# Kernel tuning notes

Hardware: AMD Instinct MI355X
Metric: run time of the kernel (lower is better)

Reference implementation:

```python
import jax, jax.numpy as jnp
import numpy as np
import math

B, S = 512, 100
L, U = 50000, 2000
D, LOC_DIM, USER_DIM, TEMP_DIM = 80, 56, 12, 12
NHEAD, DFF = 4, 160


def _pe(seq_len, d):
    pos = np.arange(seq_len, dtype=np.float32)[:, None]
    div = np.exp(np.arange(0, d, 2, dtype=np.float32) * (-math.log(10000.0) / d))
    pe = np.zeros((seq_len, d), dtype=np.float32)
    pe[:, 0::2] = np.sin(pos * div)
    pe[:, 1::2] = np.cos(pos * div)
    return jnp.asarray(pe)


def _ln(x, g, b, eps=1e-5):
    m = x.mean(-1, keepdims=True)
    v = ((x - m) ** 2).mean(-1, keepdims=True)
    return (x - m) * jax.lax.rsqrt(v + eps) * g + b


def setup_inputs():
    key = jax.random.key(0)
    ks = jax.random.split(key, 16)
    f32 = jnp.float32
    def n(k, shape, s):
        return (jax.random.normal(k, shape) * s).astype(f32)
    return {
        'loc_seq': jax.random.randint(ks[0], (B, S), 0, L),
        'user_seq': jax.random.randint(ks[1], (B, S), 0, U),
        'weekday_seq': jax.random.randint(ks[2], (B, S), 0, 7),
        'start_min_seq': (jax.random.uniform(ks[3], (B, S)) * 1440.0).astype(f32),
        'dur_seq': (jax.random.uniform(ks[4], (B, S)) * 120.0).astype(f32),
        'diff_seq': jax.random.randint(ks[5], (B, S), 0, 7),
        'mask': jnp.ones((B, S), dtype=bool),
        'loc_emb': n(ks[6], (L, LOC_DIM), 0.01).at[0].set(0.0),
        'user_emb': n(ks[7], (U, USER_DIM), 0.01).at[0].set(0.0),
        'Wt': n(ks[8], (6, TEMP_DIM), 0.3), 'bt': jnp.zeros((TEMP_DIM,), f32),
        'in_g': jnp.ones((D,), f32), 'in_b': jnp.zeros((D,), f32),
        'Wq': n(ks[9], (D, D), 0.05), 'bq': jnp.zeros((D,), f32),
        'Wk': n(ks[10], (D, D), 0.05), 'bk': jnp.zeros((D,), f32),
        'Wv': n(ks[11], (D, D), 0.05), 'bv': jnp.zeros((D,), f32),
        'Wo': n(ks[12], (D, D), 0.05), 'bo': jnp.zeros((D,), f32),
        'ln1_g': jnp.ones((D,), f32), 'ln1_b': jnp.zeros((D,), f32),
        'W1': n(ks[13], (D, DFF), 0.05), 'b1': jnp.zeros((DFF,), f32),
        'W2': n(ks[14], (DFF, D), 0.05), 'b2': jnp.zeros((D,), f32),
        'ln2_g': jnp.ones((D,), f32), 'ln2_b': jnp.zeros((D,), f32),
        'out_g': jnp.ones((D,), f32), 'out_b': jnp.zeros((D,), f32),
        'Wp': n(ks[15], (D, L), 0.05), 'bp': jnp.zeros((L,), f32),
        'recency_decay': jnp.array(0.62, f32),
        'freq_weight': jnp.array(2.2, f32),
        'history_scale': jnp.array(11.0, f32),
        'model_weight': jnp.array(0.22, f32),
    }


def reference(loc_seq, user_seq, weekday_seq, start_min_seq, dur_seq, diff_seq, mask,
              loc_emb, user_emb, Wt, bt, in_g, in_b,
              Wq, bq, Wk, bk, Wv, bv, Wo, bo, ln1_g, ln1_b,
              W1, b1, W2, b2, ln2_g, ln2_b, out_g, out_b, Wp, bp,
              recency_decay, freq_weight, history_scale, model_weight):
    b, s = loc_seq.shape
    nloc = Wp.shape[1]
    valid = mask.astype(jnp.float32)
    # --- history scores: the torch per-timestep scatter loop, vectorized ---
    t = jnp.arange(s)
    rec_w = recency_decay ** (s - 1 - t).astype(jnp.float32)      # (s,) decay^time_from_end
    bidx = jnp.broadcast_to(jnp.arange(b)[:, None], (b, s))
    recency = jnp.zeros((b, nloc), jnp.float32).at[bidx, loc_seq].max(rec_w[None, :] * valid)
    freq = jnp.zeros((b, nloc), jnp.float32).at[bidx, loc_seq].add(valid)
    freq = freq / jnp.maximum(freq.max(axis=1, keepdims=True), 1.0)
    history_scores = history_scale * (recency + freq_weight * freq)
    # --- embeddings & temporal features ---
    time_rad = start_min_seq / 60.0 / 24.0 * 2.0 * math.pi
    wd_rad = weekday_seq.astype(jnp.float32) / 7.0 * 2.0 * math.pi
    feats = jnp.stack([jnp.sin(time_rad), jnp.cos(time_rad), jnp.log1p(dur_seq) / 8.0,
                       jnp.sin(wd_rad), jnp.cos(wd_rad), diff_seq.astype(jnp.float32) / 7.0], axis=-1)
    x = jnp.concatenate([loc_emb[loc_seq], user_emb[user_seq], feats @ Wt + bt], axis=-1)
    x = _ln(x, in_g, in_b) + _pe(s, x.shape[-1])[None]
    # --- 1-layer post-norm transformer encoder, erf-gelu, eval (no dropout) ---
    dh = D // NHEAD
    q = (x @ Wq + bq).reshape(b, s, NHEAD, dh)
    k = (x @ Wk + bk).reshape(b, s, NHEAD, dh)
    v = (x @ Wv + bv).reshape(b, s, NHEAD, dh)
    scores = jnp.einsum('bqhd,bkhd->bhqk', q, k) / math.sqrt(dh)
    scores = jnp.where(mask[:, None, None, :], scores, -1e9)
    attn = jnp.einsum('bhqk,bkhd->bqhd', jax.nn.softmax(scores, axis=-1), v).reshape(b, s, D)
    x = _ln(x + attn @ Wo + bo, ln1_g, ln1_b)
    x = _ln(x + jax.nn.gelu(x @ W1 + b1, approximate=False) @ W2 + b2, ln2_g, ln2_b)
    # --- gather last valid position ---
    last_idx = mask.sum(axis=1) - 1
    last = jnp.take_along_axis(x, last_idx[:, None, None], axis=1)[:, 0]
    last = _ln(last, out_g, out_b)
    learned = jax.nn.softmax(last @ Wp + bp, axis=1) * nloc
    return history_scores + model_weight * learned
```

## Files before the change

kernel.cpp:

```cpp
#include <hip/hip_runtime.h>
#include <hip/hip_bf16.h>
#include <math.h>

#define B 512
#define S 100
#define L 50000
#define D 80
#define NHEAD 4
#define DH 20
#define DFF 160
#define NTOK (B*S)
#define NTILES 3125

typedef __attribute__((ext_vector_type(8))) short bf16x8v;
typedef __attribute__((ext_vector_type(4))) float f32x4v;
typedef __attribute__((ext_vector_type(4))) unsigned short u16x4;
typedef __attribute__((ext_vector_type(8))) unsigned short u16x8;

__device__ __forceinline__ unsigned short f2bf(float f) {
    unsigned int x = __float_as_uint(f);
    unsigned int r = (x + 0x7FFFu + ((x >> 16) & 1u)) >> 16;
    return (unsigned short)r;
}

__device__ __forceinline__ float bf2f(unsigned short u) {
    return __uint_as_float(((unsigned int)u) << 16);
}

__device__ __forceinline__ float pe_val(int s, int d) {
    int k = d >> 1;
    float ang = (float)s * expf(-0.23025850929940458f * (float)k);
    return (d & 1) ? cosf(ang) : sinf(ang);
}

__global__ __launch_bounds__(256) void pack_all(const float* __restrict__ Wq, const float* __restrict__ Wk,
                        const float* __restrict__ Wv, const float* __restrict__ Wo,
                        const float* __restrict__ W1, const float* __restrict__ W2,
                        unsigned short* __restrict__ U) {
    int bid = blockIdx.x;
    const float* W; int K, N, KT, nt; unsigned short* dst;
    if (bid < 15)      { int mt = bid / 5; nt = bid % 5; W = (mt==0)?Wq:(mt==1)?Wk:Wv; K=80; N=80; KT=3; dst = U + (size_t)bid * 1536; }
    else if (bid < 20) { nt = bid - 15; W = Wo; K=80;  N=80;  KT=3; dst = U + 23040 + (size_t)nt * 1536; }
    else if (bid < 30) { nt = bid - 20; W = W1; K=80;  N=160; KT=3; dst = U + 30720 + (size_t)nt * 1536; }
    else               { nt = bid - 30; W = W2; K=160; N=80;  KT=5; dst = U + 46080 + (size_t)nt * 2560; }
    int total = KT * 512;
    for (int idx = threadIdx.x; idx < total; idx += 256) {
        int j = idx & 7, n = (idx >> 3) & 15, q = (idx >> 7) & 3, kt = idx >> 9;
        int k = kt * 32 + q * 8 + j;
        float val = (k < K) ? W[(size_t)k * N + nt * 16 + n] : 0.f;
        dst[idx] = f2bf(val);
    }
}

__global__ __launch_bounds__(256) void build_x(const int* __restrict__ loc_seq, const int* __restrict__ user_seq,
                        const int* __restrict__ weekday_seq, const float* __restrict__ start_min,
                        const float* __restrict__ dur, const int* __restrict__ diff,
                        const float* __restrict__ loc_emb, const float* __restrict__ user_emb,
                        const float* __restrict__ Wt, const float* __restrict__ bt,
                        const float* __restrict__ in_g, const float* __restrict__ in_b,
                        unsigned short* __restrict__ x) {
    int token = blockIdx.x * 4 + (threadIdx.x >> 6);
    int lane = threadIdx.x & 63;
    int s = token % S;
    int lidx = loc_seq[token];
    int uidx = user_seq[token];
    float tr = start_min[token] * (2.f * (float)M_PI / 1440.f);
    float wd = (float)weekday_seq[token] * (2.f * (float)M_PI / 7.f);
    float f0 = sinf(tr), f1 = cosf(tr);
    float f2 = log1pf(dur[token]) * 0.125f;
    float f3 = sinf(wd), f4 = cosf(wd);
    float f5 = (float)diff[token] * (1.f / 7.f);
    float v1;
    if (lane < 56) v1 = loc_emb[(size_t)lidx * 56 + lane];
    else           v1 = user_emb[(size_t)uidx * 12 + (lane - 56)];
    float v2 = 0.f;
    if (lane < 4) {
        v2 = user_emb[(size_t)uidx * 12 + 8 + lane];
    } else if (lane < 16) {
        int j = lane - 4;
        v2 = bt[j] + f0 * Wt[j] + f1 * Wt[12 + j] + f2 * Wt[24 + j]
                   + f3 * Wt[36 + j] + f4 * Wt[48 + j] + f5 * Wt[60 + j];
    }
    float sum = v1 + v2, sq = v1 * v1 + v2 * v2;
    #pragma unroll
    for (int off = 1; off < 64; off <<= 1) {
        sum += __shfl_xor(sum, off);
        sq  += __shfl_xor(sq,  off);
    }
    float mean = sum * 0.0125f;
    float var = sq * 0.0125f - mean * mean;
    float rstd = rsqrtf(var + 1e-5f);
    x[(size_t)token * D + lane] = f2bf((v1 - mean) * rstd * in_g[lane] + in_b[lane] + pe_val(s, lane));
    if (lane < 16) {
        int d2 = 64 + lane;
        x[(size_t)token * D + d2] = f2bf((v2 - mean) * rstd * in_g[d2] + in_b[d2] + pe_val(s, d2));
    }
}

__global__ __launch_bounds__(256) void qkv_attn_fused(const unsigned short* __restrict__ xg,
      const unsigned short* __restrict__ qkvP,
      const float* __restrict__ bq, const float* __restrict__ bk, const float* __restrict__ bv,
      unsigned short* __restrict__ ao) {
    __shared__ __align__(16) unsigned short qls[128 * 128];
    __shared__ __align__(16) unsigned short kls[112 * 128];
    __shared__ __align__(16) unsigned short vt[4 * 32 * 128];
    __shared__ __align__(16) unsigned short pqk[128 * 128];
    int tid = threadIdx.x;
    int b = blockIdx.x;
    unsigned short* xbf = pqk;
    size_t base = (size_t)b * (S * D);
    f32x4v zz = {0.f, 0.f, 0.f, 0.f};
    f32x4v* q4 = (f32x4v*)qls; f32x4v* k4 = (f32x4v*)kls; f32x4v* v4 = (f32x4v*)vt;
    #pragma unroll
    for (int ii = 0; ii < 8; ++ii) q4[tid + ii * 256] = zz;
    #pragma unroll
    for (int ii = 0; ii < 7; ++ii) k4[tid + ii * 256] = zz;
    #pragma unroll
    for (int ii = 0; ii < 8; ++ii) v4[tid + ii * 256] = zz;
    #pragma unroll
    for (int ii = 0; ii < 8; ++ii) {
        int i = tid + ii * 256;
        if (i < 2000) {
            int row = i / 20, c0 = (i % 20) * 4;
            *(u16x4*)&xbf[row * 96 + c0] = *(const u16x4*)&xg[base + row * 80 + c0];
        }
    }
    unsigned int* xb32 = (unsigned int*)xbf;
    for (int i = tid; i < 576; i += 256) xb32[4800 + i] = 0;
    for (int i = tid; i < 800; i += 256) { int r = i / 8, c = i % 8; xb32[r * 48 + 40 + c] = 0; }
    __syncthreads();
    int w = tid >> 6, lane = tid & 63;
    int qd = lane >> 4, m = lane & 15;
    for (int mt = w; mt < 7; mt += 4) {
        bf16x8v a[3];
        #pragma unroll
        for (int t = 0; t < 3; ++t)
            a[t] = *(const bf16x8v*)&xbf[(mt * 16 + m) * 96 + t * 32 + qd * 8];
        #pragma unroll
        for (int nt = 0; nt < 15; ++nt) {
            f32x4v acc = {0.f, 0.f, 0.f, 0.f};
            #pragma unroll
            for (int t = 0; t < 3; ++t) {
                bf16x8v bb = *(const bf16x8v*)&qkvP[(((size_t)(nt * 3 + t)) * 4 + qd) * 128 + m * 8];
                acc = __builtin_amdgcn_mfma_f32_16x16x32_bf16(a[t], bb, acc, 0, 0, 0);
            }
            int mat = nt / 5;
            int col80 = nt * 16 + m - mat * 80;
            int h = col80 / 20, dd = col80 % 20;
            const float* bias = (mat == 0) ? bq : (mat == 1) ? bk : bv;
            float bbv = bias[col80];
            float scl = (mat == 0) ? 0.22360679774997896f : 1.f;
            #pragma unroll
            for (int r = 0; r < 4; ++r) {
                int row = mt * 16 + qd * 4 + r;
                unsigned short val = f2bf((acc[r] + bbv) * scl);
                if (mat == 0)      qls[row * 128 + ((h * 32 + dd) ^ ((row & 7) << 3))] = val;
                else if (mat == 1) kls[row * 128 + ((h * 32 + dd) ^ ((row & 7) << 3))] = val;
                else               vt[h * 4096 + dd * 128 + (row ^ ((dd & 7) << 3))] = val;
            }
        }
    }
    __syncthreads();
    #pragma unroll
    for (int ii = 0; ii < 2; ++ii) {
        int i = tid + ii * 256;
        int row = i >> 2, j = (i & 3) * 4;
        u16x4 zp = {0, 0, 0, 0};
        *(u16x4*)&pqk[row * 128 + ((112 + j) ^ ((row & 7) << 3))] = zp;
    }
    f32x4v os[4][2][2];
    #pragma unroll
    for (int h = 0; h < 4; ++h) {
        int hb = h * 32;
        bf16x8v aq[2];
        #pragma unroll
        for (int mt2 = 0; mt2 < 2; ++mt2) {
            int row = (w * 2 + mt2) * 16 + m;
            aq[mt2] = *(const bf16x8v*)&qls[row * 128 + ((hb + qd * 8) ^ ((row & 7) << 3))];
        }
        f32x4v sc[2][7];
        #pragma unroll
        for (int nt = 0; nt < 7; ++nt) {
            int krow = nt * 16 + m;
            bf16x8v bk_ = *(const bf16x8v*)&kls[krow * 128 + ((hb + qd * 8) ^ ((krow & 7) << 3))];
            #pragma unroll
            for (int mt2 = 0; mt2 < 2; ++mt2) {
                f32x4v z = {0.f, 0.f, 0.f, 0.f};
                sc[mt2][nt] = __builtin_amdgcn_mfma_f32_16x16x32_bf16(aq[mt2], bk_, z, 0, 0, 0);
            }
        }
        float inv_l[2][4];
        #pragma unroll
        for (int mt2 = 0; mt2 < 2; ++mt2) {
            #pragma unroll
            for (int r = 0; r < 4; ++r) {
                float mx = sc[mt2][0][r];
                #pragma unroll
                for (int nt = 1; nt < 6; ++nt) mx = fmaxf(mx, sc[mt2][nt][r]);
                float s6 = sc[mt2][6][r];
                if (m < 4) mx = fmaxf(mx, s6);
                #pragma unroll
                for (int off = 1; off < 16; off <<= 1) mx = fmaxf(mx, __shfl_xor(mx, off));
                float l = 0.f;
                #pragma unroll
                for (int nt = 0; nt < 6; ++nt) {
                    float p = expf(sc[mt2][nt][r] - mx);
                    sc[mt2][nt][r] = p; l += p;
                }
                float p6 = (m < 4) ? expf(s6 - mx) : 0.f;
                sc[mt2][6][r] = p6; l += p6;
                #pragma unroll
                for (int off = 1; off < 16; off <<= 1) l += __shfl_xor(l, off);
                inv_l[mt2][r] = 1.f / l;
            }
        }
        __syncthreads();
        #pragma unroll
        for (int mt2 = 0; mt2 < 2; ++mt2) {
            #pragma unroll
            for (int r = 0; r < 4; ++r) {
                int row = (w * 2 + mt2) * 16 + qd * 4 + r;
                int sw = (row & 7) << 3;
                #pragma unroll
                for (int nt = 0; nt < 7; ++nt)
                    pqk[row * 128 + ((nt * 16 + m) ^ sw)] = f2bf(sc[mt2][nt][r]);
            }
        }
        __syncthreads();
        #pragma unroll
        for (int mt2 = 0; mt2 < 2; ++mt2)
            #pragma unroll
            for (int nt2 = 0; nt2 < 2; ++nt2) { f32x4v z = {0.f,0.f,0.f,0.f}; os[h][mt2][nt2] = z; }
        #pragma unroll
        for (int kt = 0; kt < 4; ++kt) {
            int ksw = (m & 7) << 3;
            bf16x8v bv0 = *(const bf16x8v*)&vt[h * 4096 + (m) * 128 + ((kt * 32 + qd * 8) ^ ksw)];
            bf16x8v bv1 = *(const bf16x8v*)&vt[h * 4096 + (16 + m) * 128 + ((kt * 32 + qd * 8) ^ ksw)];
            #pragma unroll
            for (int mt2 = 0; mt2 < 2; ++mt2) {
                int row = (w * 2 + mt2) * 16 + m;
                bf16x8v pa = *(const bf16x8v*)&pqk[row * 128 + ((kt * 32 + qd * 8) ^ ksw)];
                os[h][mt2][0] = __builtin_amdgcn_mfma_f32_16x16x32_bf16(pa, bv0, os[h][mt2][0], 0, 0, 0);
                os[h][mt2][1] = __builtin_amdgcn_mfma_f32_16x16x32_bf16(pa, bv1, os[h][mt2][1], 0, 0, 0);
            }
        }
        #pragma unroll
        for (int mt2 = 0; mt2 < 2; ++mt2)
            #pragma unroll
            for (int r = 0; r < 4; ++r) {
                os[h][mt2][0][r] *= inv_l[mt2][r];
                os[h][mt2][1][r] *= inv_l[mt2][r];
            }
    }
    __syncthreads();
    unsigned short* aols = pqk;
    #pragma unroll
    for (int h = 0; h < 4; ++h) {
        #pragma unroll
        for (int mt2 = 0; mt2 < 2; ++mt2) {
            #pragma unroll
            for (int r = 0; r < 4; ++r) {
                int row = (w * 2 + mt2) * 16 + qd * 4 + r;
                aols[row * 96 + h * 20 + m] = f2bf(os[h][mt2][0][r]);
                if (m < 4) aols[row * 96 + h * 20 + 16 + m] = f2bf(os[h][mt2][1][r]);
            }
        }
    }
    __syncthreads();
    #pragma unroll
    for (int ii = 0; ii < 4; ++ii) {
        int i = tid + ii * 256;
        if (i < 1000) {
            int row = i / 10, c = (i % 10) * 8;
            *(u16x8*)&ao[base + row * 80 + c] = *(u16x8*)&aols[row * 96 + c];
        }
    }
}

__global__ __launch_bounds__(256) void encoder_tail(const unsigned short* __restrict__ aog,
      const unsigned short* __restrict__ xg,
      const unsigned short* __restrict__ woP, const float* __restrict__ bo,
      const float* __restrict__ ln1g, const float* __restrict__ ln1b,
      const unsigned short* __restrict__ w1P, const float* __restrict__ b1,
      const unsigned short* __restrict__ w2P, const float* __restrict__ b2,
      const float* __restrict__ ln2g, const float* __restrict__ ln2b,
      const float* __restrict__ outg, const float* __restrict__ outb,
      unsigned short* __restrict__ apack) {
    __shared__ unsigned short ubuf[64 * 160];
    __shared__ unsigned short xbf[64 * 96];
    __shared__ float ys[64 * 84];
    __shared__ float rsum[64][4], rsq[64][4];
    __shared__ float mstat[64], rstat[64];
    int tid = threadIdx.x;
    size_t base = (size_t)blockIdx.x * 64 * D;
    #pragma unroll
    for (int ii = 0; ii < 5; ++ii) {
        int i = tid + ii * 256;
        int row = i / 20, c0 = (i % 20) * 4;
        *(u16x4*)&ubuf[row * 96 + c0] = *(const u16x4*)&aog[base + row * 80 + c0];
        u16x4 xv = *(const u16x4*)&xg[base + row * 80 + c0];
        f32x4v xf;
        #pragma unroll
        for (int j = 0; j < 4; ++j) xf[j] = bf2f(xv[j]);
        *(f32x4v*)&ys[row * 84 + c0] = xf;
    }
    #pragma unroll
    for (int ii = 0; ii < 2; ++ii) {
        int i = tid + ii * 256;
        int row = i >> 3, c = i & 7;
        ((unsigned int*)ubuf)[row * 48 + 40 + c] = 0;
    }
    __syncthreads();
    int w = tid >> 6, lane = tid & 63;
    int qd = lane >> 4, m = lane & 15;
    {
        bf16x8v a[3];
        #pragma unroll
        for (int t = 0; t < 3; ++t)
            a[t] = *(const bf16x8v*)&ubuf[(w * 16 + m) * 96 + t * 32 + qd * 8];
        #pragma unroll
        for (int nt = 0; nt < 5; ++nt) {
            f32x4v acc = {0.f, 0.f, 0.f, 0.f};
            #pragma unroll
            for (int t = 0; t < 3; ++t) {
                bf16x8v b = *(const bf16x8v*)&woP[(((size_t)(nt * 3 + t)) * 4 + qd) * 128 + m * 8];
                acc = __builtin_amdgcn_mfma_f32_16x16x32_bf16(a[t], b, acc, 0, 0, 0);
            }
            int col = nt * 16 + m;
            float bbv = bo[col];
            #pragma unroll
            for (int r = 0; r < 4; ++r)
                ys[(w * 16 + qd * 4 + r) * 84 + col] += acc[r] + bbv;
        }
    }
    __syncthreads();
    {
        int row = tid >> 2, qq = tid & 3;
        float s = 0.f, sq = 0.f;
        #pragma unroll
        for (int j = 0; j < 20; ++j) { float v = ys[row * 84 + qq + 4 * j]; s += v; sq += v * v; }
        rsum[row][qq] = s; rsq[row][qq] = sq;
    }
    __syncthreads();
    if (tid < 64) {
        float s = rsum[tid][0] + rsum[tid][1] + rsum[tid][2] + rsum[tid][3];
        float sq = rsq[tid][0] + rsq[tid][1] + rsq[tid][2] + rsq[tid][3];
        float mean = s * 0.0125f;
        float var = sq * 0.0125f - mean * mean;
        mstat[tid] = mean; rstat[tid] = rsqrtf(var + 1e-5f);
    }
    __syncthreads();
    for (int idx = tid; idx < 64 * 96; idx += 256) {
        int row = idx / 96, kk = idx % 96;
        float val = 0.f;
        if (kk < D) {
            val = (ys[row * 84 + kk] - mstat[row]) * rstat[row] * ln1g[kk] + ln1b[kk];
            ys[row * 84 + kk] = val;
        }
        xbf[idx] = f2bf(val);
    }
    __syncthreads();
    {
        bf16x8v a[3];
        #pragma unroll
        for (int t = 0; t < 3; ++t)
            a[t] = *(const bf16x8v*)&xbf[(w * 16 + m) * 96 + t * 32 + qd * 8];
        #pragma unroll
        for (int nt = 0; nt < 10; ++nt) {
            f32x4v acc = {0.f, 0.f, 0.f, 0.f};
            #pragma unroll
            for (int t = 0; t < 3; ++t) {
                bf16x8v b = *(const bf16x8v*)&w1P[(((size_t)(nt * 3 + t)) * 4 + qd) * 128 + m * 8];
                acc = __builtin_amdgcn_mfma_f32_16x16x32_bf16(a[t], b, acc, 0, 0, 0);
            }
            int col = nt * 16 + m;
            float bbv = b1[col];
            #pragma unroll
            for (int r = 0; r < 4; ++r) {
                float aa = acc[r] + bbv;
                float gl = 0.5f * aa * (1.f + erff(aa * 0.70710678118654752f));
                ubuf[(w * 16 + qd * 4 + r) * 160 + col] = f2bf(gl);
            }
        }
    }
    __syncthreads();
    {
        bf16x8v a2[5];
        #pragma unroll
        for (int t = 0; t < 5; ++t)
            a2[t] = *(const bf16x8v*)&ubuf[(w * 16 + m) * 160 + t * 32 + qd * 8];
        #pragma unroll
        for (int nt = 0; nt < 5; ++nt) {
            f32x4v acc = {0.f, 0.f, 0.f, 0.f};
            #pragma unroll
            for (int t = 0; t < 5; ++t) {
                bf16x8v b = *(const bf16x8v*)&w2P[(((size_t)(nt * 5 + t)) * 4 + qd) * 128 + m * 8];
                acc = __builtin_amdgcn_mfma_f32_16x16x32_bf16(a2[t], b, acc, 0, 0, 0);
            }
            int col = nt * 16 + m;
            float bbv = b2[col];
            #pragma unroll
            for (int r = 0; r < 4; ++r)
                ys[(w * 16 + qd * 4 + r) * 84 + col] += acc[r] + bbv;
        }
    }
    __syncthreads();
    {
        int row = tid >> 2, qq = tid & 3;
        float s = 0.f, sq = 0.f;
        #pragma unroll
        for (int j = 0; j < 20; ++j) { float v = ys[row * 84 + qq + 4 * j]; s += v; sq += v * v; }
        rsum[row][qq] = s; rsq[row][qq] = sq;
    }
    __syncthreads();
    if (tid < 64) {
        float s = rsum[tid][0] + rsum[tid][1] + rsum[tid][2] + rsum[tid][3];
        float sq = rsq[tid][0] + rsq[tid][1] + rsq[tid][2] + rsq[tid][3];
        float mean = s * 0.0125f;
        float var = sq * 0.0125f - mean * mean;
        mstat[tid] = mean; rstat[tid] = rsqrtf(var + 1e-5f);
    }
    __syncthreads();
    int t0 = blockIdx.x * 64;
    int srow = (99 - (t0 % 100)) % 100;
    if (srow < 64) {
        float* lastrow = (float*)rsum;
        if (tid < 80)
            lastrow[tid] = (ys[srow * 84 + tid] - mstat[srow]) * rstat[srow] * ln2g[tid] + ln2b[tid];
        __syncthreads();
        if (tid < 64) {
            float v1 = lastrow[tid];
            float v2 = (tid < 16) ? lastrow[64 + tid] : 0.f;
            float sum = v1 + v2, sq = v1 * v1 + v2 * v2;
            #pragma unroll
            for (int off = 1; off < 64; off <<= 1) {
                sum += __shfl_xor(sum, off);
                sq  += __shfl_xor(sq,  off);
            }
            float mean = sum * 0.0125f;
            float var = sq * 0.0125f - mean * mean;
            float rstd = rsqrtf(var + 1e-5f);
            int bb = (t0 + srow) / 100;
            int mtile = bb >> 4, mm = bb & 15;
            {
                int d = tid;
                float val = (v1 - mean) * rstd * outg[d] + outb[d];
                int t = d >> 5, q = (d & 31) >> 3, j = d & 7;
                apack[((((size_t)mtile * 3 + t) * 4 + q) * 16 + mm) * 8 + j] = f2bf(val);
            }
            if (tid < 32) {
                int d = 64 + tid;
                float val = (tid < 16) ? ((v2 - mean) * rstd * outg[d] + outb[d]) : 0.f;
                int t = d >> 5, q = (d & 31) >> 3, j = d & 7;
                apack[((((size_t)mtile * 3 + t) * 4 + q) * 16 + mm) * 8 + j] = f2bf(val);
            }
        }
    }
}

__global__ __launch_bounds__(256) void wp_pack(const float* __restrict__ Wp, unsigned short* __restrict__ bpack,
                                               float* __restrict__ rowsum) {
    int tid = threadIdx.x;
    int nt = blockIdx.x;
    if (nt == 0) { rowsum[tid] = 0.f; rowsum[256 + tid] = 0.f; }
    for (int idx = tid; idx < 1536; idx += 256) {
        int n = idx & 15, kk = idx >> 4;
        int t = kk >> 5, q = (kk & 31) >> 3, j = kk & 7;
        float val = (kk < D) ? Wp[(size_t)kk * L + nt * 16 + n] : 0.f;
        bpack[((((size_t)nt * 3 + t) * 4 + q) * 16 + n) * 8 + j] = f2bf(val);
    }
}

__global__ __launch_bounds__(256) void rowsum_mfma(const unsigned short* __restrict__ apack,
                                                   const unsigned short* __restrict__ bpack,
                                                   const float* __restrict__ bp,
                                                   float* __restrict__ rowsum) {
    __shared__ float part[4][512];
    int tid = threadIdx.x;
    int w = tid >> 6, lane = tid & 63;
    int q = lane >> 4, m = lane & 15;
    int nt0 = (blockIdx.x * 4 + w) * 4;
    const bf16x8v* BP = (const bf16x8v*)bpack;
    const bf16x8v* AP = (const bf16x8v*)apack;
    bf16x8v bfr[4][3];
    float bpv[4], liv[4];
    #pragma unroll
    for (int i = 0; i < 4; ++i) {
        int ntile = nt0 + i;
        int ntc = ntile < NTILES ? ntile : NTILES - 1;
        liv[i] = ntile < NTILES ? 1.f : 0.f;
        #pragma unroll
        for (int t = 0; t < 3; ++t)
            bfr[i][t] = BP[((size_t)ntc * 3 + t) * 64 + q * 16 + m];
        bpv[i] = bp[ntc * 16 + m];
    }
    for (int mt = 0; mt < 32; ++mt) {
        bf16x8v a[3];
        #pragma unroll
        for (int t = 0; t < 3; ++t) a[t] = AP[((size_t)mt * 3 + t) * 64 + q * 16 + m];
        float rs[4] = {0.f, 0.f, 0.f, 0.f};
        #pragma unroll
        for (int i = 0; i < 4; ++i) {
            f32x4v acc = {0.f, 0.f, 0.f, 0.f};
            #pragma unroll
            for (int t = 0; t < 3; ++t)
                acc = __builtin_amdgcn_mfma_f32_16x16x32_bf16(a[t], bfr[i][t], acc, 0, 0, 0);
            #pragma unroll
            for (int r = 0; r < 4; ++r) rs[r] += liv[i] * expf(acc[r] + bpv[i]);
        }
        #pragma unroll
        for (int r = 0; r < 4; ++r) {
            #pragma unroll
            for (int off = 1; off < 16; off <<= 1) rs[r] += __shfl_xor(rs[r], off);
        }
        if (m == 0) {
            #pragma unroll
            for (int r = 0; r < 4; ++r) part[w][mt * 16 + q * 4 + r] = rs[r];
        }
    }
    __syncthreads();
    for (int i = tid; i < 512; i += 256) {
        float s = part[0][i] + part[1][i] + part[2][i] + part[3][i];
        atomicAdd(&rowsum[i], s);
    }
}

__global__ __launch_bounds__(256) void logits_final(const unsigned short* __restrict__ apack,
      const unsigned short* __restrict__ bpack, const float* __restrict__ bp,
      const float* __restrict__ rowsum, const float* __restrict__ mwp,
      float* __restrict__ out) {
    __shared__ float tile[2][16][68];
    __shared__ float sc[512];
    int tid = threadIdx.x;
    int w = tid >> 6, lane = tid & 63;
    int q = lane >> 4, m = lane & 15;
    float mwL = mwp[0] * (float)L;
    for (int i = tid; i < 512; i += 256) sc[i] = mwL / rowsum[i];
    int ntile = blockIdx.x * 4 + w;
    int ntc = ntile < NTILES ? ntile : NTILES - 1;
    bool live = ntile < NTILES;
    const bf16x8v* BP = (const bf16x8v*)bpack;
    const bf16x8v* AP = (const bf16x8v*)apack;
    bf16x8v bfr[3];
    #pragma unroll
    for (int t = 0; t < 3; ++t) bfr[t] = BP[((size_t)ntc * 3 + t) * 64 + q * 16 + m];
    float bpv = bp[ntc * 16 + m];
    int row = tid >> 4, c4 = tid & 15;
    int gc = blockIdx.x * 64 + c4 * 4;
    bool cok = gc + 4 <= L;
    bf16x8v aC[3], aN[3];
    #pragma unroll
    for (int t = 0; t < 3; ++t) aC[t] = AP[(size_t)t * 64 + q * 16 + m];
    __syncthreads();
    for (int mt = 0; mt < 32; ++mt) {
        if (mt < 31) {
            #pragma unroll
            for (int t = 0; t < 3; ++t) aN[t] = AP[((size_t)(mt + 1) * 3 + t) * 64 + q * 16 + m];
        }
        f32x4v acc = {0.f, 0.f, 0.f, 0.f};
        #pragma unroll
        for (int t = 0; t < 3; ++t)
            acc = __builtin_amdgcn_mfma_f32_16x16x32_bf16(aC[t], bfr[t], acc, 0, 0, 0);
        int buf = mt & 1;
        if (live) {
            #pragma unroll
            for (int r = 0; r < 4; ++r)
                tile[buf][q * 4 + r][w * 16 + m] = expf(acc[r] + bpv);
        }
        __syncthreads();
        if (cok) {
            float4 v = *(float4*)&tile[buf][row][c4 * 4];
            float s = sc[mt * 16 + row];
            v.x *= s; v.y *= s; v.z *= s; v.w *= s;
            *(float4*)&out[(size_t)(mt * 16 + row) * L + gc] = v;
        }
        #pragma unroll
        for (int t = 0; t < 3; ++t) aC[t] = aN[t];
    }
}

__global__ void history_kern(const int* __restrict__ loc_seq, const float* __restrict__ decp,
                             const float* __restrict__ fwp, const float* __restrict__ hsp,
                             float* __restrict__ out) {
    int b = blockIdx.x;
    int t = threadIdx.x;
    __shared__ int locs[S];
    __shared__ float red[128];
    if (t < S) locs[t] = loc_seq[(size_t)b * S + t];
    __syncthreads();
    int cnt = 0;
    bool isLast = false;
    int myloc = -1;
    if (t < S) {
        myloc = locs[t];
        isLast = true;
        for (int u = 0; u < S; ++u) {
            if (locs[u] == myloc) { cnt++; if (u > t) isLast = false; }
        }
    }
    red[t] = (float)cnt;
    __syncthreads();
    for (int off = 64; off; off >>= 1) { if (t < off) red[t] = fmaxf(red[t], red[t + off]); __syncthreads(); }
    float denom = fmaxf(red[0], 1.0f);
    if (t < S && isLast) {
        float rec = powf(decp[0], (float)(S - 1 - t));
        out[(size_t)b * L + myloc] += hsp[0] * (rec + fwp[0] * (float)cnt / denom);
    }
}

extern "C" void kernel_launch(void* const* d_in, const int* in_sizes, int n_in,
                              void* d_out, int out_size, void* d_ws, size_t ws_size,
                              hipStream_t stream) {
    (void)in_sizes; (void)n_in; (void)out_size; (void)ws_size;
    const int*   loc_seq   = (const int*)  d_in[0];
    const int*   user_seq  = (const int*)  d_in[1];
    const int*   weekday   = (const int*)  d_in[2];
    const float* start_min = (const float*)d_in[3];
    const float* dur       = (const float*)d_in[4];
    const int*   diff      = (const int*)  d_in[5];
    const float* loc_emb = (const float*)d_in[7];
    const float* user_emb= (const float*)d_in[8];
    const float* Wt  = (const float*)d_in[9];  const float* bt  = (const float*)d_in[10];
    const float* in_g= (const float*)d_in[11]; const float* in_b= (const float*)d_in[12];
    const float* Wq  = (const float*)d_in[13]; const float* bq  = (const float*)d_in[14];
    const float* Wk  = (const float*)d_in[15]; const float* bk  = (const float*)d_in[16];
    const float* Wv  = (const float*)d_in[17]; const float* bv  = (const float*)d_in[18];
    const float* Wo  = (const float*)d_in[19]; const float* bo  = (const float*)d_in[20];
    const float* ln1g= (const float*)d_in[21]; const float* ln1b= (const float*)d_in[22];
    const float* W1  = (const float*)d_in[23]; const float* b1  = (const float*)d_in[24];
    const float* W2  = (const float*)d_in[25]; const float* b2  = (const float*)d_in[26];
    const float* ln2g= (const float*)d_in[27]; const float* ln2b= (const float*)d_in[28];
    const float* outg= (const float*)d_in[29]; const float* outb= (const float*)d_in[30];
    const float* Wp  = (const float*)d_in[31]; const float* bp  = (const float*)d_in[32];
    const float* dec = (const float*)d_in[33]; const float* fw  = (const float*)d_in[34];
    const float* hs  = (const float*)d_in[35]; const float* mw  = (const float*)d_in[36];

    float* ws   = (float*)d_ws;
    unsigned short* Xb = (unsigned short*)ws;
    unsigned short* APACK = (unsigned short*)(ws + 4096000);
    unsigned short* AO = (unsigned short*)(ws + 16384000);
    float* RSUM = ws + 20480000;
    unsigned short* WPACKS = (unsigned short*)(ws + 20481000);
    unsigned short* QKVP = WPACKS;
    unsigned short* WOP  = WPACKS + 23040;
    unsigned short* W1P  = WPACKS + 30720;
    unsigned short* W2P  = WPACKS + 46080;
    unsigned short* BPACK = AO;
    float* out  = (float*)d_out;

    pack_all<<<35, 256, 0, stream>>>(Wq, Wk, Wv, Wo, W1, W2, WPACKS);
    build_x<<<NTOK / 4, 256, 0, stream>>>(loc_seq, user_seq, weekday, start_min, dur, diff,
                                          loc_emb, user_emb, Wt, bt, in_g, in_b, Xb);
    qkv_attn_fused<<<B, 256, 0, stream>>>(Xb, QKVP, bq, bk, bv, AO);
    encoder_tail<<<NTOK / 64, 256, 0, stream>>>(AO, Xb, WOP, bo, ln1g, ln1b,
                                                W1P, b1, W2P, b2, ln2g, ln2b,
                                                outg, outb, APACK);
    wp_pack<<<NTILES, 256, 0, stream>>>(Wp, BPACK, RSUM);
    rowsum_mfma<<<(NTILES + 15) / 16, 256, 0, stream>>>(APACK, BPACK, bp, RSUM);
    logits_final<<<(NTILES + 3) / 4, 256, 0, stream>>>(APACK, BPACK, bp, RSUM, mw, out);
    history_kern<<<B, 128, 0, stream>>>(loc_seq, dec, fw, hs, out);
}
```

Measured before the change: 387.1 us.

## Double attention block to 512 threads with one query tile per wave

Raises the fused QKV+attention kernel to 512 threads (8 waves), so each wave handles one 16-row query tile instead of two, and each of the first 7 waves computes a single QKV projection row tile. This shortens each wave's serial work and its register footprint within a block. The cost is more waves contending for the same LDS budget, an idle eighth wave during the projection, and possibly lower occupancy per CU given the large shared memory per block.

```diff
diff --git a/kernel.cpp b/kernel.cpp
--- a/kernel.cpp
+++ b/kernel.cpp
@@ -97,7 +97,7 @@
     }
 }
 
-__global__ __launch_bounds__(256) void qkv_attn_fused(const unsigned short* __restrict__ xg,
+__global__ __launch_bounds__(512) void qkv_attn_fused(const unsigned short* __restrict__ xg,
       const unsigned short* __restrict__ qkvP,
       const float* __restrict__ bq, const float* __restrict__ bk, const float* __restrict__ bv,
       unsigned short* __restrict__ ao) {
@@ -112,26 +112,27 @@
     f32x4v zz = {0.f, 0.f, 0.f, 0.f};
     f32x4v* q4 = (f32x4v*)qls; f32x4v* k4 = (f32x4v*)kls; f32x4v* v4 = (f32x4v*)vt;
     #pragma unroll
-    for (int ii = 0; ii < 8; ++ii) q4[tid + ii * 256] = zz;
-    #pragma unroll
-    for (int ii = 0; ii < 7; ++ii) k4[tid + ii * 256] = zz;
-    #pragma unroll
-    for (int ii = 0; ii < 8; ++ii) v4[tid + ii * 256] = zz;
-    #pragma unroll
-    for (int ii = 0; ii < 8; ++ii) {
-        int i = tid + ii * 256;
+    for (int ii = 0; ii < 4; ++ii) q4[tid + ii * 512] = zz;
+    #pragma unroll
+    for (int ii = 0; ii < 4; ++ii) { int i = tid + ii * 512; if (i < 1792) k4[i] = zz; }
+    #pragma unroll
+    for (int ii = 0; ii < 4; ++ii) v4[tid + ii * 512] = zz;
+    #pragma unroll
+    for (int ii = 0; ii < 4; ++ii) {
+        int i = tid + ii * 512;
         if (i < 2000) {
             int row = i / 20, c0 = (i % 20) * 4;
             *(u16x4*)&xbf[row * 96 + c0] = *(const u16x4*)&xg[base + row * 80 + c0];
         }
     }
     unsigned int* xb32 = (unsigned int*)xbf;
-    for (int i = tid; i < 576; i += 256) xb32[4800 + i] = 0;
-    for (int i = tid; i < 800; i += 256) { int r = i / 8, c = i % 8; xb32[r * 48 + 40 + c] = 0; }
+    for (int i = tid; i < 576; i += 512) xb32[4800 + i] = 0;
+    for (int i = tid; i < 800; i += 512) { int r = i / 8, c = i % 8; xb32[r * 48 + 40 + c] = 0; }
     __syncthreads();
     int w = tid >> 6, lane = tid & 63;
     int qd = lane >> 4, m = lane & 15;
-    for (int mt = w; mt < 7; mt += 4) {
+    if (w < 7) {
+        int mt = w;
         bf16x8v a[3];
         #pragma unroll
         for (int t = 0; t < 3; ++t)
@@ -161,115 +162,91 @@
         }
     }
     __syncthreads();
-    #pragma unroll
-    for (int ii = 0; ii < 2; ++ii) {
-        int i = tid + ii * 256;
+    {
+        int i = tid;
         int row = i >> 2, j = (i & 3) * 4;
         u16x4 zp = {0, 0, 0, 0};
         *(u16x4*)&pqk[row * 128 + ((112 + j) ^ ((row & 7) << 3))] = zp;
     }
-    f32x4v os[4][2][2];
+    f32x4v os[4][2];
     #pragma unroll
     for (int h = 0; h < 4; ++h) {
         int hb = h * 32;
-        bf16x8v aq[2];
-        #pragma unroll
-        for (int mt2 = 0; mt2 < 2; ++mt2) {
-            int row = (w * 2 + mt2) * 16 + m;
-            aq[mt2] = *(const bf16x8v*)&qls[row * 128 + ((hb + qd * 8) ^ ((row & 7) << 3))];
-        }
-        f32x4v sc[2][7];
+        int rowq = w * 16 + m;
+        bf16x8v aq = *(const bf16x8v*)&qls[rowq * 128 + ((hb + qd * 8) ^ ((rowq & 7) << 3))];
+        f32x4v sc[7];
         #pragma unroll
         for (int nt = 0; nt < 7; ++nt) {
             int krow = nt * 16 + m;
             bf16x8v bk_ = *(const bf16x8v*)&kls[krow * 128 + ((hb + qd * 8) ^ ((krow & 7) << 3))];
-            #pragma unroll
-            for (int mt2 = 0; mt2 < 2; ++mt2) {
-                f32x4v z = {0.f, 0.f, 0.f, 0.f};
-                sc[mt2][nt] = __builtin_amdgcn_mfma_f32_16x16x32_bf16(aq[mt2], bk_, z, 0, 0, 0);
-            }
-        }
-        float inv_l[2][4];
-        #pragma unroll
-        for (int mt2 = 0; mt2 < 2; ++mt2) {
-            #pragma unroll
-            for (int r = 0; r < 4; ++r) {
-                float mx = sc[mt2][0][r];
-                #pragma unroll
-                for (int nt = 1; nt < 6; ++nt) mx = fmaxf(mx, sc[mt2][nt][r]);
-                float s6 = sc[mt2][6][r];
-                if (m < 4) mx = fmaxf(mx, s6);
-                #pragma unroll
-                for (int off = 1; off < 16; off <<= 1) mx = fmaxf(mx, __shfl_xor(mx, off));
-                float l = 0.f;
-                #pragma unroll
-                for (int nt = 0; nt < 6; ++nt) {
-                    float p = expf(sc[mt2][nt][r] - mx);
-                    sc[mt2][nt][r] = p; l += p;
-                }
-                float p6 = (m < 4) ? expf(s6 - mx) : 0.f;
-                sc[mt2][6][r] = p6; l += p6;
-                #pragma unroll
-                for (int off = 1; off < 16; off <<= 1) l += __shfl_xor(l, off);
-                inv_l[mt2][r] = 1.f / l;
-            }
+            f32x4v z = {0.f, 0.f, 0.f, 0.f};
+            sc[nt] = __builtin_amdgcn_mfma_f32_16x16x32_bf16(aq, bk_, z, 0, 0, 0);
+        }
+        float inv_l[4];
+        #pragma unroll
+        for (int r = 0; r < 4; ++r) {
+            float mx = sc[0][r];
+            #pragma unroll
+            for (int nt = 1; nt < 6; ++nt) mx = fmaxf(mx, sc[nt][r]);
+            float s6 = sc[6][r];
+            if (m < 4) mx = fmaxf(mx, s6);
+            #pragma unroll
+            for (int off = 1; off < 16; off <<= 1) mx = fmaxf(mx, __shfl_xor(mx, off));
+            float l = 0.f;
+            #pragma unroll
+            for (int nt = 0; nt < 6; ++nt) {
+                float p = expf(sc[nt][r] - mx);
+                sc[nt][r] = p; l += p;
+            }
+            float p6 = (m < 4) ? expf(s6 - mx) : 0.f;
+            sc[6][r] = p6; l += p6;
+            #pragma unroll
+            for (int off = 1; off < 16; off <<= 1) l += __shfl_xor(l, off);
+            inv_l[r] = 1.f / l;
         }
         __syncthreads();
         #pragma unroll
-        for (int mt2 = 0; mt2 < 2; ++mt2) {
-            #pragma unroll
-            for (int r = 0; r < 4; ++r) {
-                int row = (w * 2 + mt2) * 16 + qd * 4 + r;
-                int sw = (row & 7) << 3;
-                #pragma unroll
-                for (int nt = 0; nt < 7; ++nt)
-                    pqk[row * 128 + ((nt * 16 + m) ^ sw)] = f2bf(sc[mt2][nt][r]);
-            }
+        for (int r = 0; r < 4; ++r) {
+            int row = w * 16 + qd * 4 + r;
+            int sw = (row & 7) << 3;
+            #pragma unroll
+            for (int nt = 0; nt < 7; ++nt)
+                pqk[row * 128 + ((nt * 16 + m) ^ sw)] = f2bf(sc[nt][r]);
         }
         __syncthreads();
         #pragma unroll
-        for (int mt2 = 0; mt2 < 2; ++mt2)
-            #pragma unroll
-            for (int nt2 = 0; nt2 < 2; ++nt2) { f32x4v z = {0.f,0.f,0.f,0.f}; os[h][mt2][nt2] = z; }
+        for (int nt2 = 0; nt2 < 2; ++nt2) { f32x4v z = {0.f,0.f,0.f,0.f}; os[h][nt2] = z; }
         #pragma unroll
         for (int kt = 0; kt < 4; ++kt) {
             int ksw = (m & 7) << 3;
             bf16x8v bv0 = *(const bf16x8v*)&vt[h * 4096 + (m) * 128 + ((kt * 32 + qd * 8) ^ ksw)];
             bf16x8v bv1 = *(const bf16x8v*)&vt[h * 4096 + (16 + m) * 128 + ((kt * 32 + qd * 8) ^ ksw)];
-            #pragma unroll
-            for (int mt2 = 0; mt2 < 2; ++mt2) {
-                int row = (w * 2 + mt2) * 16 + m;
-                bf16x8v pa = *(const bf16x8v*)&pqk[row * 128 + ((kt * 32 + qd * 8) ^ ksw)];
-                os[h][mt2][0] = __builtin_amdgcn_mfma_f32_16x16x32_bf16(pa, bv0, os[h][mt2][0], 0, 0, 0);
-                os[h][mt2][1] = __builtin_amdgcn_mfma_f32_16x16x32_bf16(pa, bv1, os[h][mt2][1], 0, 0, 0);
-            }
-        }
-        #pragma unroll
-        for (int mt2 = 0; mt2 < 2; ++mt2)
-            #pragma unroll
-            for (int r = 0; r < 4; ++r) {
-                os[h][mt2][0][r] *= inv_l[mt2][r];
-                os[h][mt2][1][r] *= inv_l[mt2][r];
-            }
+            int row = w * 16 + m;
+            bf16x8v pa = *(const bf16x8v*)&pqk[row * 128 + ((kt * 32 + qd * 8) ^ ksw)];
+            os[h][0] = __builtin_amdgcn_mfma_f32_16x16x32_bf16(pa, bv0, os[h][0], 0, 0, 0);
+            os[h][1] = __builtin_amdgcn_mfma_f32_16x16x32_bf16(pa, bv1, os[h][1], 0, 0, 0);
+        }
+        #pragma unroll
+        for (int r = 0; r < 4; ++r) {
+            os[h][0][r] *= inv_l[r];
+            os[h][1][r] *= inv_l[r];
+        }
     }
     __syncthreads();
     unsigned short* aols = pqk;
     #pragma unroll
     for (int h = 0; h < 4; ++h) {
         #pragma unroll
-        for (int mt2 = 0; mt2 < 2; ++mt2) {
-            #pragma unroll
-            for (int r = 0; r < 4; ++r) {
-                int row = (w * 2 + mt2) * 16 + qd * 4 + r;
-                aols[row * 96 + h * 20 + m] = f2bf(os[h][mt2][0][r]);
-                if (m < 4) aols[row * 96 + h * 20 + 16 + m] = f2bf(os[h][mt2][1][r]);
-            }
-        }
-    }
-    __syncthreads();
-    #pragma unroll
-    for (int ii = 0; ii < 4; ++ii) {
-        int i = tid + ii * 256;
+        for (int r = 0; r < 4; ++r) {
+            int row = w * 16 + qd * 4 + r;
+            aols[row * 96 + h * 20 + m] = f2bf(os[h][0][r]);
+            if (m < 4) aols[row * 96 + h * 20 + 16 + m] = f2bf(os[h][1][r]);
+        }
+    }
+    __syncthreads();
+    #pragma unroll
+    for (int ii = 0; ii < 2; ++ii) {
+        int i = tid + ii * 512;
         if (i < 1000) {
             int row = i / 10, c = (i % 10) * 8;
             *(u16x8*)&ao[base + row * 80 + c] = *(u16x8*)&aols[row * 96 + c];
@@ -651,7 +628,7 @@
     pack_all<<<35, 256, 0, stream>>>(Wq, Wk, Wv, Wo, W1, W2, WPACKS);
     build_x<<<NTOK / 4, 256, 0, stream>>>(loc_seq, user_seq, weekday, start_min, dur, diff,
                                           loc_emb, user_emb, Wt, bt, in_g, in_b, Xb);
-    qkv_attn_fused<<<B, 256, 0, stream>>>(Xb, QKVP, bq, bk, bv, AO);
+    qkv_attn_fused<<<B, 512, 0, stream>>>(Xb, QKVP, bq, bk, bv, AO);
     encoder_tail<<<NTOK / 64, 256, 0, stream>>>(AO, Xb, WOP, bo, ln1g, ln1b,
                                                 W1P, b1, W2P, b2, ln2g, ln2b,
                                                 outg, outb, APACK);
```

After: 372.3 us. 1.04x faster.
